# Kernel optimization log

Hardware: AMD Instinct MI355X
Metric: run time of the kernel (lower is better)

The kernel has to match this reference:

```python
import jax, jax.numpy as jnp
import numpy as np

B, N, N_UP = 4096, 16, 8          # walkers, electrons, up-spin electrons
D1, D2 = 256, 32                  # single-stream / double-stream widths
FLEN = 3 * D1 + 2 * D2            # f-vector length (both spins present)


def setup_inputs() -> dict:
    key = jax.random.key(0)
    k = jax.random.split(key, 6)
    return {
        "single_h": jax.random.normal(k[0], (B, N, D1), dtype=jnp.float32),
        "double_h": jax.random.normal(k[1], (B, N, N, D2), dtype=jnp.float32),
        # learned params (torch.rand -> uniform[0,1))
        "v_matrices": jax.random.uniform(k[2], (N, FLEN, D1), dtype=jnp.float32),
        "b_vectors": jax.random.uniform(k[3], (N, D1), dtype=jnp.float32),
        "w_matrices": jax.random.uniform(k[4], (N, N, D2, D2), dtype=jnp.float32),
        "c_vectors": jax.random.uniform(k[5], (N, N, D2), dtype=jnp.float32),
        "n_up": N_UP,
    }


def reference(single_h, double_h, v_matrices, b_vectors, w_matrices, c_vectors, n_up):
    # spin-resolved mean pools
    g_up = jnp.mean(single_h[:, :n_up], axis=1)        # (B, D1)
    g_dn = jnp.mean(single_h[:, n_up:], axis=1)        # (B, D1)
    dg_up = jnp.mean(double_h[:, :, :n_up], axis=2)    # (B, N, D2)
    dg_dn = jnp.mean(double_h[:, :, n_up:], axis=2)    # (B, N, D2)

    # f_vectors: concat(single_h[i], g_up, g_dn, dg_up[i], dg_dn[i]) -> (B, N, FLEN)
    f = jnp.concatenate([
        single_h,
        jnp.broadcast_to(g_up[:, None, :], single_h.shape),
        jnp.broadcast_to(g_dn[:, None, :], single_h.shape),
        dg_up,
        dg_dn,
    ], axis=-1)

    # per-electron linear: v[i]^T @ f[i] + b[i], tanh, residual (shapes match by construction)
    single_out = jnp.tanh(jnp.einsum('bnf,nfo->bno', f, v_matrices) + b_vectors)
    single_out = single_out + single_h

    # per-pair linear: w[i,j] @ h[i,j] + c[i,j] (bmm contracts over w's last axis), tanh, residual
    double_out = jnp.tanh(jnp.einsum('ijde,bije->bijd', w_matrices, double_h) + c_vectors)
    double_out = double_out + double_h

    return single_out, double_out
```

## Files before the change

kernel.cpp:

```cpp
#include <hip/hip_runtime.h>


#define NWALK 4096
#define NEL   16
#define D1V   256
#define D2V   32

typedef short  bf16x8 __attribute__((ext_vector_type(8)));
typedef float  f32x4  __attribute__((ext_vector_type(4)));
typedef unsigned short u16;

__device__ __forceinline__ float tanh_fast(float x) {
  return 1.0f - 2.0f / (__expf(2.0f * x) + 1.0f);
}
__device__ __forceinline__ u16 bf16_rne(float f) {
  unsigned u = __float_as_uint(f);
  unsigned r = (u + 0x7FFFu + ((u >> 16) & 1u)) >> 16;
  return (u16)r;
}
__device__ __forceinline__ float bf16_to_f(u16 h) {
  return __uint_as_float(((unsigned)h) << 16);
}
__device__ __forceinline__ void gload_lds16(const void* g, void* l) {
  __builtin_amdgcn_global_load_lds(
      (const __attribute__((address_space(1))) void*)g,
      (__attribute__((address_space(3))) void*)l, 16, 0, 0);
}

__global__ __launch_bounds__(256) void k_pool_g(const float* __restrict__ sh,
                                                float* __restrict__ gup,
                                                float* __restrict__ gdn) {
  int idx = blockIdx.x * 256 + threadIdx.x;
  int b = idx >> 8;
  int d = idx & 255;
  const float* p = sh + (size_t)b * (NEL * D1V) + d;
  float su = 0.f, sd = 0.f;
#pragma unroll
  for (int n = 0; n < 8; ++n) su += p[n * D1V];
#pragma unroll
  for (int n = 8; n < 16; ++n) sd += p[n * D1V];
  gup[idx] = su * 0.125f;
  gdn[idx] = sd * 0.125f;
}

__global__ __launch_bounds__(256) void k_pool_dg(const float* __restrict__ dh,
                                                 float* __restrict__ dgup,
                                                 float* __restrict__ dgdn) {
  int idx = blockIdx.x * 256 + threadIdx.x;
  int b = idx >> 9;
  int r = idx & 511;
  const float* p = dh + (size_t)b * 8192 + (size_t)(r >> 5) * 512 + (r & 31);
  float su = 0.f, sd = 0.f;
#pragma unroll
  for (int j = 0; j < 8; ++j) su += p[j * 32];
#pragma unroll
  for (int j = 8; j < 16; ++j) sd += p[j * 32];
  dgup[idx] = su * 0.125f;
  dgdn[idx] = sd * 0.125f;
}

__global__ __launch_bounds__(256) void k_vsplit(const float* __restrict__ v,
                                                u16* __restrict__ vs) {
  int nb = blockIdx.x;
  int n = nb / 26, kt = nb - n * 26;
  int col = threadIdx.x;
  const float* src = v + ((size_t)n * 832 + (size_t)kt * 32) * 256 + col;
  u16* hb = vs + (size_t)nb * 16384;
  u16* lb = hb + 8192;
  int sw = (col >> 1) & 3;
#pragma unroll
  for (int cp = 0; cp < 4; ++cp) {
    int ks = cp ^ sw;
    bf16x8 hi, lo;
#pragma unroll
    for (int j = 0; j < 8; ++j) {
      float f = src[(size_t)(ks * 8 + j) * 256];
      u16 h = bf16_rne(f);
      hi[j] = (short)h;
      lo[j] = (short)bf16_rne(f - bf16_to_f(h));
    }
    *(bf16x8*)(hb + col * 32 + cp * 8) = hi;
    *(bf16x8*)(lb + col * 32 + cp * 8) = lo;
  }
}

__global__ __launch_bounds__(256, 2) void k_single(
    const float* __restrict__ sh, const u16* __restrict__ vs,
    const float* __restrict__ bvec, const float* __restrict__ gup,
    const float* __restrict__ gdn, const float* __restrict__ dgup,
    const float* __restrict__ dgdn, float* __restrict__ out) {
  __shared__ alignas(16) short A2[2][128][32];
  __shared__ alignas(16) short V2[2][256][32];
  const int t = threadIdx.x;
  const int bid = blockIdx.x;
  const int n = bid >> 5;
  const int b0 = (bid & 31) * 128;
  const int lane = t & 63;
  const int w = t >> 6;
  const int wr = w >> 1, wc = w & 1;
  const int l15 = lane & 15, l4 = lane >> 4;

  const int arow = wr * 64 + l15;
  const int aslot = l4 ^ ((arow >> 1) & 3);
  const int aoff = arow * 32 + aslot * 8;
  const int bcol = wc * 128 + l15;
  const int bslot = l4 ^ ((bcol >> 1) & 3);
  const int boff = bcol * 32 + bslot * 8;

  const int srow = t & 127;
  const int sc0 = t >> 7;
  const int sslot0 = sc0 ^ ((srow >> 1) & 3);
  const int sslot1 = (sc0 + 2) ^ ((srow >> 1) & 3);

  f32x4 acc[4][8];
#pragma unroll
  for (int m = 0; m < 4; ++m)
#pragma unroll
    for (int nf = 0; nf < 8; ++nf) acc[m][nf] = (f32x4){0.f, 0.f, 0.f, 0.f};

  const short* Ab = &A2[0][0][0];
  const short* Vb = &V2[0][0][0];

  for (int kt = 0; kt < 26; ++kt) {
    const float* abase;
    int rstride;
    if (kt < 8)        { abase = sh   + (size_t)b0 * 4096 + n * 256 + kt * 32;  rstride = 4096; }
    else if (kt < 16)  { abase = gup  + (size_t)b0 * 256 + (kt - 8) * 32;       rstride = 256;  }
    else if (kt < 24)  { abase = gdn  + (size_t)b0 * 256 + (kt - 16) * 32;      rstride = 256;  }
    else if (kt == 24) { abase = dgup + (size_t)b0 * 512 + n * 32;              rstride = 512;  }
    else               { abase = dgdn + (size_t)b0 * 512 + n * 32;              rstride = 512;  }

    const u16* vsrc = vs + (size_t)(n * 26 + kt) * 16384;
#pragma unroll
    for (int i = 0; i < 8; ++i) {
      gload_lds16(vsrc + (size_t)(i * 256 + t) * 8,
                  (char*)Vb + w * 1024 + i * 4096);
    }

    {
      const float* ap = abase + (size_t)srow * rstride;
      float4 x0 = *(const float4*)(ap + sc0 * 8);
      float4 x1 = *(const float4*)(ap + sc0 * 8 + 4);
      float4 y0 = *(const float4*)(ap + sc0 * 8 + 16);
      float4 y1 = *(const float4*)(ap + sc0 * 8 + 20);
      bf16x8 xh, xl, yh, yl;
      float xs[8] = {x0.x, x0.y, x0.z, x0.w, x1.x, x1.y, x1.z, x1.w};
      float ys[8] = {y0.x, y0.y, y0.z, y0.w, y1.x, y1.y, y1.z, y1.w};
#pragma unroll
      for (int j = 0; j < 8; ++j) {
        u16 h = bf16_rne(xs[j]);
        xh[j] = (short)h; xl[j] = (short)bf16_rne(xs[j] - bf16_to_f(h));
        u16 g = bf16_rne(ys[j]);
        yh[j] = (short)g; yl[j] = (short)bf16_rne(ys[j] - bf16_to_f(g));
      }
      *(bf16x8*)&A2[0][srow][sslot0 * 8] = xh;
      *(bf16x8*)&A2[1][srow][sslot0 * 8] = xl;
      *(bf16x8*)&A2[0][srow][sslot1 * 8] = yh;
      *(bf16x8*)&A2[1][srow][sslot1 * 8] = yl;
    }

    __syncthreads();

    bf16x8 ah[4], al[4];
#pragma unroll
    for (int m = 0; m < 4; ++m) {
      ah[m] = *(const bf16x8*)(Ab + aoff + m * 512);
      al[m] = *(const bf16x8*)(Ab + 4096 + aoff + m * 512);
    }
#pragma unroll
    for (int nf = 0; nf < 8; ++nf) {
      bf16x8 bh = *(const bf16x8*)(Vb + boff + nf * 512);
      bf16x8 bl = *(const bf16x8*)(Vb + 8192 + boff + nf * 512);
#pragma unroll
      for (int m = 0; m < 4; ++m) {
        acc[m][nf] = __builtin_amdgcn_mfma_f32_16x16x32_bf16(ah[m], bh, acc[m][nf], 0, 0, 0);
        acc[m][nf] = __builtin_amdgcn_mfma_f32_16x16x32_bf16(al[m], bh, acc[m][nf], 0, 0, 0);
        acc[m][nf] = __builtin_amdgcn_mfma_f32_16x16x32_bf16(ah[m], bl, acc[m][nf], 0, 0, 0);
      }
    }
    __syncthreads();
  }

#pragma unroll
  for (int nf = 0; nf < 8; ++nf) {
    const int col = wc * 128 + nf * 16 + l15;
    const float bias_v = bvec[n * 256 + col];
#pragma unroll
    for (int m = 0; m < 4; ++m) {
      const int brow0 = b0 + wr * 64 + m * 16 + l4 * 4;
#pragma unroll
      for (int j = 0; j < 4; ++j) {
        const size_t idx = ((size_t)(brow0 + j) * 16 + n) * 256 + col;
        out[idx] = tanh_fast(acc[m][nf][j] + bias_v) + sh[idx];
      }
    }
  }
}

__global__ __launch_bounds__(256) void k_double(const float* __restrict__ dh,
                                                const float* __restrict__ w,
                                                const float* __restrict__ c,
                                                float* __restrict__ out) {
  const int bid = blockIdx.x;
  const int pair = bid >> 4;
  const int b0 = (bid & 15) * 256;
  const int t = threadIdx.x;
  const int g = t & 15;
  const int slot = t >> 4;

  float4 w0[8], w1[8];
  const float4* wp0 = (const float4*)(w + (size_t)pair * 1024 + (2 * g) * 32);
#pragma unroll
  for (int q = 0; q < 8; ++q) { w0[q] = wp0[q]; w1[q] = wp0[q + 8]; }
  const float2 cc = *(const float2*)(c + pair * 32 + 2 * g);

  for (int it = 0; it < 16; ++it) {
    int b = b0 + it * 16 + slot;
    const size_t rowoff = (size_t)b * 8192 + (size_t)pair * 32;
    const float4* hp = (const float4*)(dh + rowoff);
    float a0 = 0.f, a1 = 0.f;
#pragma unroll
    for (int q = 0; q < 8; ++q) {
      float4 h4 = hp[q];
      a0 += w0[q].x * h4.x + w0[q].y * h4.y + w0[q].z * h4.z + w0[q].w * h4.w;
      a1 += w1[q].x * h4.x + w1[q].y * h4.y + w1[q].z * h4.z + w1[q].w * h4.w;
    }
    float2 hres = *(const float2*)(dh + rowoff + 2 * g);
    float2 o;
    o.x = tanh_fast(a0 + cc.x) + hres.x;
    o.y = tanh_fast(a1 + cc.y) + hres.y;
    *(float2*)(out + rowoff + 2 * g) = o;
  }
}

extern "C" void kernel_launch(void* const* d_in, const int* in_sizes, int n_in,
                              void* d_out, int out_size, void* d_ws, size_t ws_size,
                              hipStream_t stream) {
  const float* sh = (const float*)d_in[0];
  const float* dh = (const float*)d_in[1];
  const float* v  = (const float*)d_in[2];
  const float* bv = (const float*)d_in[3];
  const float* w  = (const float*)d_in[4];
  const float* c  = (const float*)d_in[5];
  float* out = (float*)d_out;
  (void)d_ws; (void)ws_size;

  float* out_s = out;
  float* out_d = out + 16777216;

  float* gup  = out_d;
  float* gdn  = out_d + 1048576;
  float* dgup = out_d + 2097152;
  float* dgdn = out_d + 4194304;
  u16*  vspl  = (u16*)(out_d + 6291456);

  k_pool_g <<<4096, 256, 0, stream>>>(sh, gup, gdn);
  k_pool_dg<<<8192, 256, 0, stream>>>(dh, dgup, dgdn);
  k_vsplit <<< 416, 256, 0, stream>>>(v, vspl);
  k_single <<< 512, 256, 0, stream>>>(sh, vspl, bv, gup, gdn, dgup, dgdn, out_s);
  k_double <<<4096, 256, 0, stream>>>(dh, w, c, out_d);
}
```

Measured before the change: 616.2 us.

## Stage double-stream rows in LDS and compute four outputs per thread

The double-stream kernel now stages each block's 256 walker rows for one electron pair into padded shared memory using coalesced float4 loads. Each thread then keeps four rows of the 32x32 weight matrix in registers and produces four outputs, where it previously produced two. Every walker row is read from global memory once instead of being re-read by 16 threads plus a separate residual load. The cost is heavy register pressure (128 floats of weights per thread), about 36KB of LDS per block, and a launch-bounds hint that asks for two blocks per CU.

```diff
diff --git a/kernel.cpp b/kernel.cpp
--- a/kernel.cpp
+++ b/kernel.cpp
@@ -197,39 +197,58 @@
   }
 }
 
-__global__ __launch_bounds__(256) void k_double(const float* __restrict__ dh,
-                                                const float* __restrict__ w,
-                                                const float* __restrict__ c,
-                                                float* __restrict__ out) {
+__global__ __launch_bounds__(256, 2) void k_double(const float* __restrict__ dh,
+                                                   const float* __restrict__ w,
+                                                   const float* __restrict__ c,
+                                                   float* __restrict__ out) {
+  __shared__ alignas(16) float h_lds[256][36];
   const int bid = blockIdx.x;
   const int pair = bid >> 4;
   const int b0 = (bid & 15) * 256;
   const int t = threadIdx.x;
-  const int g = t & 15;
-  const int slot = t >> 4;
-
-  float4 w0[8], w1[8];
-  const float4* wp0 = (const float4*)(w + (size_t)pair * 1024 + (2 * g) * 32);
-#pragma unroll
-  for (int q = 0; q < 8; ++q) { w0[q] = wp0[q]; w1[q] = wp0[q + 8]; }
-  const float2 cc = *(const float2*)(c + pair * 32 + 2 * g);
-
-  for (int it = 0; it < 16; ++it) {
-    int b = b0 + it * 16 + slot;
-    const size_t rowoff = (size_t)b * 8192 + (size_t)pair * 32;
-    const float4* hp = (const float4*)(dh + rowoff);
-    float a0 = 0.f, a1 = 0.f;
+  const int g = t & 7;
+  const int s = t >> 3;
+
+  float4 wr[4][8];
+  {
+    const float4* wp = (const float4*)(w + (size_t)pair * 1024 + (size_t)(g * 4) * 32);
+#pragma unroll
+    for (int d = 0; d < 4; ++d)
+#pragma unroll
+      for (int q = 0; q < 8; ++q) wr[d][q] = wp[d * 8 + q];
+  }
+  const float4 cc = *(const float4*)(c + pair * 32 + g * 4);
+
+  {
+    const int q = t & 7;
+#pragma unroll
+    for (int p = 0; p < 8; ++p) {
+      const int r = p * 32 + s;
+      const float4 hv = *(const float4*)(dh + (size_t)(b0 + r) * 8192 +
+                                         (size_t)pair * 32 + q * 4);
+      *(float4*)&h_lds[r][q * 4] = hv;
+    }
+  }
+  __syncthreads();
+
+  for (int it = 0; it < 8; ++it) {
+    const int r = it * 32 + s;
+    float4 acc = make_float4(0.f, 0.f, 0.f, 0.f);
 #pragma unroll
     for (int q = 0; q < 8; ++q) {
-      float4 h4 = hp[q];
-      a0 += w0[q].x * h4.x + w0[q].y * h4.y + w0[q].z * h4.z + w0[q].w * h4.w;
-      a1 += w1[q].x * h4.x + w1[q].y * h4.y + w1[q].z * h4.z + w1[q].w * h4.w;
-    }
-    float2 hres = *(const float2*)(dh + rowoff + 2 * g);
-    float2 o;
-    o.x = tanh_fast(a0 + cc.x) + hres.x;
-    o.y = tanh_fast(a1 + cc.y) + hres.y;
-    *(float2*)(out + rowoff + 2 * g) = o;
+      const float4 h4 = *(const float4*)&h_lds[r][q * 4];
+      acc.x += wr[0][q].x * h4.x + wr[0][q].y * h4.y + wr[0][q].z * h4.z + wr[0][q].w * h4.w;
+      acc.y += wr[1][q].x * h4.x + wr[1][q].y * h4.y + wr[1][q].z * h4.z + wr[1][q].w * h4.w;
+      acc.z += wr[2][q].x * h4.x + wr[2][q].y * h4.y + wr[2][q].z * h4.z + wr[2][q].w * h4.w;
+      acc.w += wr[3][q].x * h4.x + wr[3][q].y * h4.y + wr[3][q].z * h4.z + wr[3][q].w * h4.w;
+    }
+    const float4 hres = *(const float4*)&h_lds[r][g * 4];
+    float4 o;
+    o.x = tanh_fast(acc.x + cc.x) + hres.x;
+    o.y = tanh_fast(acc.y + cc.y) + hres.y;
+    o.z = tanh_fast(acc.z + cc.z) + hres.z;
+    o.w = tanh_fast(acc.w + cc.w) + hres.w;
+    *(float4*)(out + (size_t)(b0 + r) * 8192 + (size_t)pair * 32 + g * 4) = o;
   }
 }
 
```

After: 524.0 us. 15.0% less time.
